# Kernel optimization log

Measured on AMD Instinct MI355X. Metric: run time of the kernel, lower is better.

The kernel has to match this reference:

```python
import jax, jax.numpy as jnp
import numpy as np

D_MODEL = 512  # scale uses sqrt(d_model), faithful to source (not sqrt(d_k))


def setup_inputs() -> dict:
    key = jax.random.key(0)
    ks = jax.random.split(key, 9)
    S, H, DK, DV = 4096, 8, 128, 64
    w = lambda k, shape: jax.random.normal(k, shape, jnp.float32) * 0.02
    return {
        "x": jax.random.normal(ks[0], (S, D_MODEL), jnp.float32),
        "Wq": w(ks[1], (H, D_MODEL, DK)), "bq": w(ks[2], (H, DK)),
        "Wk": w(ks[3], (H, D_MODEL, DK)), "bk": w(ks[4], (H, DK)),
        "Wv": w(ks[5], (H, D_MODEL, DV)), "bv": w(ks[6], (H, DV)),
        "Wo": w(ks[7], (H * DV, D_MODEL)), "bo": w(ks[8], (D_MODEL,)),
    }


def reference(x, Wq, bq, Wk, bk, Wv, bv, Wo, bo):
    # Per-head Q/K/V projections, batched over heads: [H, S, dk/dv]
    q = jnp.einsum('sd,hdk->hsk', x, Wq) + bq[:, None, :]
    k = jnp.einsum('sd,hdk->hsk', x, Wk) + bk[:, None, :]
    v = jnp.einsum('sd,hdv->hsv', x, Wv) + bv[:, None, :]
    # scaled dot-product; source divides by sqrt(d_model), mask branch is a no-op
    scores = jnp.einsum('hsk,htk->hst', q, k) / jnp.sqrt(jnp.float32(D_MODEL))
    probs = jax.nn.softmax(scores, axis=-1)  # softmax(dim=1) on 2D == last axis
    heads = jnp.einsum('hst,htv->hsv', probs, v)          # [H, S, DV]
    concat = jnp.transpose(heads, (1, 0, 2)).reshape(x.shape[0], -1)  # [S, H*DV]
    return concat @ Wo + bo
```

## Files before the change

kernel.cpp:

```cpp
#include <hip/hip_runtime.h>
#include <hip/hip_bf16.h>
#include <math.h>

typedef __bf16 bf16_t;
typedef __bf16 bf16x4 __attribute__((ext_vector_type(4)));
typedef __bf16 bf16x8 __attribute__((ext_vector_type(8)));
typedef float  f32x4  __attribute__((ext_vector_type(4)));

#define LOG2E   1.4426950408889634f
#define QSCALE  0.04419417382415922f
#define QS_TOT  (QSCALE * LOG2E)

static __device__ __forceinline__ f32x4 mfma16(bf16x8 a, bf16x8 b, f32x4 c) {
    return __builtin_amdgcn_mfma_f32_16x16x32_bf16(a, b, c, 0, 0, 0);
}

static __device__ __forceinline__ void gload16(void* lds, const void* g) {
    __builtin_amdgcn_global_load_lds(
        (const __attribute__((address_space(1))) unsigned int*)g,
        (__attribute__((address_space(3))) unsigned int*)lds, 16, 0, 0);
}

__global__ void k_stage_all(const float* __restrict__ x,
                            const float* __restrict__ Wq, const float* __restrict__ Wk,
                            const float* __restrict__ Wv, const float* __restrict__ Wo,
                            const float* __restrict__ bq, const float* __restrict__ bk,
                            const float* __restrict__ bv,
                            bf16_t* __restrict__ xb, bf16_t* __restrict__ Wcat,
                            bf16_t* __restrict__ Wot, float* __restrict__ bcat) {
    __shared__ float tl[64][65];
    int b = blockIdx.x;
    if (b < 2048) {
        int i = (b * 256 + (int)threadIdx.x) * 4;
        f32x4 v = *(const f32x4*)(x + i);
        bf16x4 o;
        o[0] = (bf16_t)v[0]; o[1] = (bf16_t)v[1]; o[2] = (bf16_t)v[2]; o[3] = (bf16_t)v[3];
        *(bf16x4*)(xb + i) = o;
        return;
    }
    if (b < 2432) {
        int bb = b - 2048;
        int p = bb >> 7, bid = bb & 127;
        int h = bid >> 4, rem = bid & 15, dt = rem >> 1, ct = rem & 1;
        if (p == 2 && ct) return;
        int cols = (p == 2) ? 64 : 128;
        const float* src = (p == 0 ? Wq : (p == 1 ? Wk : Wv)) + h * 512 * cols;
        int d0 = dt * 64, c0 = ct * 64;
        int cin = threadIdx.x & 63, rb = threadIdx.x >> 6;
        #pragma unroll
        for (int j = 0; j < 16; j++) {
            int dl = rb * 16 + j;
            tl[dl][cin] = src[(d0 + dl) * cols + c0 + cin];
        }
        __syncthreads();
        float sc = (p == 0) ? QS_TOT : 1.0f;
        int nl = threadIdx.x >> 2, dch = (threadIdx.x & 3) * 16;
        int n = h * 320 + p * 128 + c0 + nl;
        bf16_t* dst = Wcat + n * 512 + d0 + dch;
        #pragma unroll
        for (int e = 0; e < 16; e += 4) {
            bf16x4 o;
            #pragma unroll
            for (int q = 0; q < 4; q++) o[q] = (bf16_t)(tl[dch + e + q][nl] * sc);
            *(bf16x4*)(dst + e) = o;
        }
        return;
    }
    if (b < 2496) {
        int bb = b - 2432;
        int r0 = (bb >> 3) * 64, c0 = (bb & 7) * 64;
        int cin = threadIdx.x & 63, rb = threadIdx.x >> 6;
        #pragma unroll
        for (int j = 0; j < 16; j++) {
            int rl = rb * 16 + j;
            tl[rl][cin] = Wo[(r0 + rl) * 512 + c0 + cin];
        }
        __syncthreads();
        int nl = threadIdx.x >> 2, dch = (threadIdx.x & 3) * 16;
        bf16_t* dst = Wot + (c0 + nl) * 512 + r0 + dch;
        #pragma unroll
        for (int e = 0; e < 16; e += 4) {
            bf16x4 o;
            #pragma unroll
            for (int q = 0; q < 4; q++) o[q] = (bf16_t)tl[dch + e + q][nl];
            *(bf16x4*)(dst + e) = o;
        }
        return;
    }
    {
        int n = (b - 2496) * 256 + (int)threadIdx.x;
        if (n >= 2560) return;
        int h = n / 320, r = n % 320;
        float v;
        if (r < 128)      v = bq[h * 128 + r] * QS_TOT;
        else if (r < 256) v = bk[h * 128 + r - 128];
        else              v = bv[h * 64 + r - 256];
        bcat[n] = v;
    }
}

static __device__ __forceinline__ void stage_tile(bf16_t* lds, const bf16_t* src_base,
                                                  int row0, int kk, int wv, int lane) {
    #pragma unroll
    for (int j = 0; j < 2; ++j) {
        int row = j * 64 + wv * 16 + (lane >> 2);
        int slot = lane & 3;
        const bf16_t* src = src_base + (size_t)(row0 + row) * 512 + kk
                          + ((slot ^ ((row >> 1) & 3)) << 3);
        gload16(lds + (j * 64 + wv * 16) * 32, src);
    }
}

__global__ __launch_bounds__(256) void k_gemm_qkv(
        const bf16_t* __restrict__ xb, const bf16_t* __restrict__ Wcat,
        const float* __restrict__ bcat,
        bf16_t* __restrict__ Qb, bf16_t* __restrict__ Kb, bf16_t* __restrict__ Vt) {
    __shared__ __align__(16) bf16_t a_lds[2][128 * 32];
    __shared__ __align__(16) bf16_t b_lds[2][128 * 32];

    int lane = threadIdx.x & 63, wv = threadIdx.x >> 6;
    int qi = lane & 15, g = lane >> 4;
    int m0 = blockIdx.x * 128;
    int n0 = blockIdx.y * 128;

    f32x4 acc[4][4];
    #pragma unroll
    for (int ar = 0; ar < 4; ar++)
        #pragma unroll
        for (int br = 0; br < 4; br++) acc[ar][br] = (f32x4){0.f,0.f,0.f,0.f};

    int arow0 = (wv >> 1) * 64;
    int brow0 = (wv & 1) * 64;

    stage_tile(&a_lds[0][0], xb,   m0, 0, wv, lane);
    stage_tile(&b_lds[0][0], Wcat, n0, 0, wv, lane);

    for (int t = 0; t < 16; ++t) {
        __syncthreads();
        int cur = t & 1;
        if (t + 1 < 16) {
            stage_tile(&a_lds[cur ^ 1][0], xb,   m0, (t + 1) * 32, wv, lane);
            stage_tile(&b_lds[cur ^ 1][0], Wcat, n0, (t + 1) * 32, wv, lane);
        }
        const char* abase = (const char*)&a_lds[cur][0];
        const char* bbase = (const char*)&b_lds[cur][0];
        bf16x8 af[4], bf[4];
        #pragma unroll
        for (int ar = 0; ar < 4; ar++) {
            int row = arow0 + ar * 16 + qi;
            af[ar] = *(const bf16x8*)(abase + row * 64 + (((g ^ (row >> 1)) & 3) << 4));
        }
        #pragma unroll
        for (int br = 0; br < 4; br++) {
            int row = brow0 + br * 16 + qi;
            bf[br] = *(const bf16x8*)(bbase + row * 64 + (((g ^ (row >> 1)) & 3) << 4));
        }
        __builtin_amdgcn_s_setprio(1);
        #pragma unroll
        for (int ar = 0; ar < 4; ar++)
            #pragma unroll
            for (int br = 0; br < 4; br++)
                acc[ar][br] = mfma16(af[ar], bf[br], acc[ar][br]);
        __builtin_amdgcn_s_setprio(0);
    }

    int mrow = m0 + arow0;
    int ncol = n0 + brow0;
    #pragma unroll
    for (int br = 0; br < 4; br++) {
        int n = ncol + br * 16 + qi;
        float bias = bcat[n];
        int h = n / 320, r = n % 320;
        #pragma unroll
        for (int ar = 0; ar < 4; ar++)
            #pragma unroll
            for (int i = 0; i < 4; i++) {
                int rr = mrow + ar * 16 + g * 4 + i;
                float val = acc[ar][br][i] + bias;
                if (r < 128)      Qb[(h * 4096 + rr) * 128 + r]         = (bf16_t)val;
                else if (r < 256) Kb[(h * 4096 + rr) * 128 + (r - 128)] = (bf16_t)val;
                else {
                    int cp = (rr & ~31) | (((rr >> 2) & 3) << 3) | (((rr >> 4) & 1) << 2) | (rr & 3);
                    Vt[(h * 64 + (r - 256)) * 4096 + cp] = (bf16_t)val;
                }
            }
    }
}

static __device__ __forceinline__ void stage_k(bf16_t* kbuf, const bf16_t* Kh,
                                               int kt, int wv, int lane) {
    #pragma unroll
    for (int j = 0; j < 4; ++j) {
        int local = wv * 16 + j * 4 + (lane >> 4);
        int physcol = (lane & 15) << 4;
        const char* src = (const char*)(Kh + (size_t)(kt + local) * 128)
                        + (physcol ^ ((local & 7) << 4));
        gload16(kbuf + (wv * 16 + j * 4) * 128, src);
    }
}

static __device__ __forceinline__ void stage_v(bf16_t* vbuf, const bf16_t* Vh,
                                               int kt, int wv, int lane) {
    #pragma unroll
    for (int jj = 0; jj < 2; ++jj) {
        int j = wv * 2 + jj;
        int dv = j * 8 + (lane >> 3);
        int slot = lane & 7;
        const bf16_t* src = Vh + (size_t)dv * 4096 + kt + ((slot ^ (dv & 7)) << 3);
        gload16(vbuf + j * 512, src);
    }
}

__global__ __launch_bounds__(256, 3) void k_attn(
        const bf16_t* __restrict__ Qb, const bf16_t* __restrict__ Kb,
        const bf16_t* __restrict__ Vt, bf16_t* __restrict__ Cb,
        float* __restrict__ Opart, float* __restrict__ Lpart) {
    __shared__ __align__(16) bf16_t k_lds[2][64 * 128];
    __shared__ __align__(16) bf16_t v_lds[2][64 * 64];

    const int lane = threadIdx.x & 63, wv = threadIdx.x >> 6;
    const int qi = lane & 15, g = lane >> 4;

    int nwg = 32 * 8 * gridDim.z, cpx = nwg >> 3;
    int wgid = blockIdx.x + 32 * (blockIdx.y + 8 * blockIdx.z);
    int wk = (wgid & 7) * cpx + (wgid >> 3);
    const int qb = wk & 31, h = (wk >> 5) & 7, split = wk >> 8;

    const int nsplits = gridDim.z;
    const int tbase = 64 / nsplits, trem = 64 % nsplits;
    const int tstart = split * tbase + (split < trem ? split : trem);
    const int ntiles = tbase + (split < trem ? 1 : 0);

    const int q0 = qb * 128 + wv * 32;
    int rot = (int)(((unsigned)wgid * 2654435761u) >> 24) % ntiles;

    const bf16_t* Qh = Qb + h * 4096 * 128;
    const bf16_t* Kh = Kb + h * 4096 * 128;
    const bf16_t* Vh = Vt + h * 64 * 4096;

    bf16x8 qf[2][4];
    #pragma unroll
    for (int qt = 0; qt < 2; qt++)
        #pragma unroll
        for (int c = 0; c < 4; c++)
            qf[qt][c] = *(const bf16x8*)(Qh + (q0 + qt * 16 + qi) * 128 + c * 32 + g * 8);

    float l[2] = {0.f, 0.f};
    f32x4 oacc[2][4];
    #pragma unroll
    for (int qt = 0; qt < 2; qt++)
        #pragma unroll
        for (int c = 0; c < 4; c++) oacc[qt][c] = (f32x4){0.f,0.f,0.f,0.f};

    {
        int kt0 = (tstart + rot) * 64;
        stage_k(&k_lds[0][0], Kh, kt0, wv, lane);
        stage_v(&v_lds[0][0], Vh, kt0, wv, lane);
    }
    __syncthreads();

    for (int ii = 0; ii < ntiles; ++ii) {
        const int cur = ii & 1;
        if (ii + 1 < ntiles) {
            int idn = ii + 1 + rot; if (idn >= ntiles) idn -= ntiles;
            int ktn = (tstart + idn) * 64;
            stage_k(&k_lds[cur ^ 1][0], Kh, ktn, wv, lane);
            stage_v(&v_lds[cur ^ 1][0], Vh, ktn, wv, lane);
        }

        f32x4 s[2][4];
        #pragma unroll
        for (int qt = 0; qt < 2; qt++)
            #pragma unroll
            for (int t = 0; t < 4; t++) s[qt][t] = (f32x4){0.f,0.f,0.f,0.f};
        __builtin_amdgcn_s_setprio(1);
        #pragma unroll
        for (int t = 0; t < 4; t++) {
            const bf16_t* kr = &k_lds[cur][(t * 16 + qi) * 128];
            #pragma unroll
            for (int c = 0; c < 4; c++) {
                int offb = (c * 64 + g * 16) ^ ((qi & 7) << 4);
                bf16x8 kf = *(const bf16x8*)(kr + (offb >> 1));
                s[0][t] = mfma16(kf, qf[0][c], s[0][t]);
                s[1][t] = mfma16(kf, qf[1][c], s[1][t]);
            }
        }
        __builtin_amdgcn_s_setprio(0);

        float p[2][4][4];
        #pragma unroll
        for (int qt = 0; qt < 2; qt++) {
            float ks = 0.f;
            #pragma unroll
            for (int t = 0; t < 4; t++)
                #pragma unroll
                for (int i = 0; i < 4; i++) {
                    float e = __builtin_amdgcn_exp2f(s[qt][t][i]);
                    p[qt][t][i] = e;
                    ks += e;
                }
            l[qt] += ks;
        }

        bf16x8 pb[2][2];
        #pragma unroll
        for (int qt = 0; qt < 2; qt++)
            #pragma unroll
            for (int u = 0; u < 2; u++) {
                bf16x8 t8;
                #pragma unroll
                for (int e = 0; e < 4; e++) {
                    t8[e]     = (bf16_t)p[qt][2 * u][e];
                    t8[4 + e] = (bf16_t)p[qt][2 * u + 1][e];
                }
                pb[qt][u] = t8;
            }

        __builtin_amdgcn_s_setprio(1);
        #pragma unroll
        for (int c = 0; c < 4; c++) {
            const char* vrow = (const char*)&v_lds[cur][0] + (c * 16 + qi) * 128;
            #pragma unroll
            for (int u = 0; u < 2; u++) {
                int offb = (g * 16 + u * 64) ^ ((qi & 7) << 4);
                bf16x8 vf = *(const bf16x8*)(vrow + offb);
                oacc[0][c] = mfma16(vf, pb[0][u], oacc[0][c]);
                oacc[1][c] = mfma16(vf, pb[1][u], oacc[1][c]);
            }
        }
        __builtin_amdgcn_s_setprio(0);

        __syncthreads();
    }

    #pragma unroll
    for (int qt = 0; qt < 2; qt++) {
        l[qt] += __shfl_xor(l[qt], 16);
        l[qt] += __shfl_xor(l[qt], 32);
    }

    if (gridDim.z == 1) {
        #pragma unroll
        for (int qt = 0; qt < 2; qt++) {
            float inv = 1.0f / l[qt];
            int q = q0 + qt * 16 + qi;
            #pragma unroll
            for (int c = 0; c < 4; c++) {
                bf16x4 o4;
                #pragma unroll
                for (int i = 0; i < 4; i++) o4[i] = (bf16_t)(oacc[qt][c][i] * inv);
                *(bf16x4*)(Cb + q * 512 + h * 64 + c * 16 + g * 4) = o4;
            }
        }
    } else {
        #pragma unroll
        for (int qt = 0; qt < 2; qt++) {
            int q = q0 + qt * 16 + qi;
            float* Op = Opart + ((size_t)(split * 8 + h) * 4096 + q) * 64;
            #pragma unroll
            for (int c = 0; c < 4; c++)
                *(f32x4*)(Op + c * 16 + g * 4) = oacc[qt][c];
            if (g == 0)
                Lpart[(size_t)(split * 8 + h) * 4096 + q] = l[qt];
        }
    }
}

__global__ void k_merge(const float* __restrict__ Opart, const float* __restrict__ Lpart,
                        bf16_t* __restrict__ Cb, int splits) {
    int idx = blockIdx.x * 256 + threadIdx.x;
    int q = idx >> 7, rem = idx & 127;
    int hv4 = rem * 4;
    int h = hv4 >> 6, dv = hv4 & 63;

    f32x4 acc = {0.f, 0.f, 0.f, 0.f};
    float L = 0.f;
    for (int s = 0; s < splits; s++) {
        L += Lpart[(size_t)(s * 8 + h) * 4096 + q];
        f32x4 ov = *(const f32x4*)(Opart + ((size_t)(s * 8 + h) * 4096 + q) * 64 + dv);
        #pragma unroll
        for (int e = 0; e < 4; e++) acc[e] += ov[e];
    }
    float inv = 1.0f / L;
    bf16x4 o4;
    #pragma unroll
    for (int e = 0; e < 4; e++) o4[e] = (bf16_t)(acc[e] * inv);
    *(bf16x4*)(Cb + (size_t)q * 512 + hv4) = o4;
}

__global__ __launch_bounds__(256) void k_gemm_out(
        const bf16_t* __restrict__ Cb, const bf16_t* __restrict__ Wot,
        const float* __restrict__ bo, float* __restrict__ out) {
    __shared__ __align__(16) bf16_t a_lds[2][128 * 32];
    __shared__ __align__(16) bf16_t b_lds[2][128 * 32];

    int lane = threadIdx.x & 63, wv = threadIdx.x >> 6;
    int qi = lane & 15, g = lane >> 4;
    int m0 = blockIdx.x * 128;
    int n0 = blockIdx.y * 128;

    f32x4 acc[4][4];
    #pragma unroll
    for (int ar = 0; ar < 4; ar++)
        #pragma unroll
        for (int br = 0; br < 4; br++) acc[ar][br] = (f32x4){0.f,0.f,0.f,0.f};

    int arow0 = (wv >> 1) * 64;
    int brow0 = (wv & 1) * 64;

    stage_tile(&a_lds[0][0], Cb,  m0, 0, wv, lane);
    stage_tile(&b_lds[0][0], Wot, n0, 0, wv, lane);

    for (int t = 0; t < 16; ++t) {
        __syncthreads();
        int cur = t & 1;
        if (t + 1 < 16) {
            stage_tile(&a_lds[cur ^ 1][0], Cb,  m0, (t + 1) * 32, wv, lane);
            stage_tile(&b_lds[cur ^ 1][0], Wot, n0, (t + 1) * 32, wv, lane);
        }
        const char* abase = (const char*)&a_lds[cur][0];
        const char* bbase = (const char*)&b_lds[cur][0];
        bf16x8 af[4], bf[4];
        #pragma unroll
        for (int ar = 0; ar < 4; ar++) {
            int row = arow0 + ar * 16 + qi;
            af[ar] = *(const bf16x8*)(abase + row * 64 + (((g ^ (row >> 1)) & 3) << 4));
        }
        #pragma unroll
        for (int br = 0; br < 4; br++) {
            int row = brow0 + br * 16 + qi;
            bf[br] = *(const bf16x8*)(bbase + row * 64 + (((g ^ (row >> 1)) & 3) << 4));
        }
        __builtin_amdgcn_s_setprio(1);
        #pragma unroll
        for (int ar = 0; ar < 4; ar++)
            #pragma unroll
            for (int br = 0; br < 4; br++)
                acc[ar][br] = mfma16(af[ar], bf[br], acc[ar][br]);
        __builtin_amdgcn_s_setprio(0);
    }

    int mrow = m0 + arow0;
    int ncol = n0 + brow0;
    #pragma unroll
    for (int br = 0; br < 4; br++) {
        int n = ncol + br * 16 + qi;
        float bias = bo[n];
        #pragma unroll
        for (int ar = 0; ar < 4; ar++)
            #pragma unroll
            for (int i = 0; i < 4; i++)
                out[(mrow + ar * 16 + g * 4 + i) * 512 + n] = acc[ar][br][i] + bias;
    }
}

extern "C" void kernel_launch(void* const* d_in, const int* in_sizes, int n_in,
                              void* d_out, int out_size, void* d_ws, size_t ws_size,
                              hipStream_t stream) {
    const float* x  = (const float*)d_in[0];
    const float* Wq = (const float*)d_in[1];
    const float* bq = (const float*)d_in[2];
    const float* Wk = (const float*)d_in[3];
    const float* bk = (const float*)d_in[4];
    const float* Wv = (const float*)d_in[5];
    const float* bv = (const float*)d_in[6];
    const float* Wo = (const float*)d_in[7];
    const float* bo = (const float*)d_in[8];
    float* out = (float*)d_out;

    char* ws = (char*)d_ws;
    bf16_t* xb    = (bf16_t*)(ws + 0);
    bf16_t* Wcat  = (bf16_t*)(ws + 4194304);
    bf16_t* Qb    = (bf16_t*)(ws + 6815744);
    bf16_t* Kb    = (bf16_t*)(ws + 15204352);
    bf16_t* Vt    = (bf16_t*)(ws + 23592960);
    bf16_t* Cb    = (bf16_t*)(ws + 27787264);
    bf16_t* Wot   = (bf16_t*)(ws + 31981568);
    float*  bcat  = (float*)(ws + 32505856);
    float*  Opart = (float*)(ws + 32516096);
    float*  Lprt  = (float*)(ws + 57681920);
    const size_t NEED3 = 58075136;
    int splits = (ws_size >= NEED3) ? 3 : 1;

    hipLaunchKernelGGL(k_stage_all,  dim3(2506),   dim3(256), 0, stream,
                       x, Wq, Wk, Wv, Wo, bq, bk, bv, xb, Wcat, Wot, bcat);
    hipLaunchKernelGGL(k_gemm_qkv,   dim3(32, 20), dim3(256), 0, stream, xb, Wcat, bcat, Qb, Kb, Vt);
    hipLaunchKernelGGL(k_attn,       dim3(32, 8, splits), dim3(256), 0, stream, Qb, Kb, Vt, Cb, Opart, Lprt);
    if (splits > 1)
        hipLaunchKernelGGL(k_merge,  dim3(2048),   dim3(256), 0, stream, Opart, Lprt, Cb, splits);
    hipLaunchKernelGGL(k_gemm_out,   dim3(32, 4),  dim3(256), 0, stream, Cb, Wot, bo, out);
}
```

Measured before the change: 110.9 us.

## Single-buffer V tile to fit four attention blocks per CU, use four KV splits

V staging in the attention kernel goes from double-buffered to single-buffered, which cuts LDS per block. That lets the launch bound rise from 3 to 4 blocks per CU. V fragments are now read into registers before an added barrier, and the next V tile is loaded afterwards, overlapping with the PV MFMAs. The host uses four KV splits when the workspace is large enough and moves the partial-L buffer to make room. The cost is an extra barrier per tile, less prefetch depth for V, and more partial results to merge.

```diff
diff --git a/kernel.cpp b/kernel.cpp
--- a/kernel.cpp
+++ b/kernel.cpp
@@ -211,12 +211,12 @@
     }
 }
 
-__global__ __launch_bounds__(256, 3) void k_attn(
+__global__ __launch_bounds__(256, 4) void k_attn(
         const bf16_t* __restrict__ Qb, const bf16_t* __restrict__ Kb,
         const bf16_t* __restrict__ Vt, bf16_t* __restrict__ Cb,
         float* __restrict__ Opart, float* __restrict__ Lpart) {
     __shared__ __align__(16) bf16_t k_lds[2][64 * 128];
-    __shared__ __align__(16) bf16_t v_lds[2][64 * 64];
+    __shared__ __align__(16) bf16_t v_lds[64 * 64];
 
     const int lane = threadIdx.x & 63, wv = threadIdx.x >> 6;
     const int qi = lane & 15, g = lane >> 4;
@@ -255,17 +255,18 @@
     {
         int kt0 = (tstart + rot) * 64;
         stage_k(&k_lds[0][0], Kh, kt0, wv, lane);
-        stage_v(&v_lds[0][0], Vh, kt0, wv, lane);
+        stage_v(&v_lds[0], Vh, kt0, wv, lane);
     }
     __syncthreads();
 
     for (int ii = 0; ii < ntiles; ++ii) {
         const int cur = ii & 1;
-        if (ii + 1 < ntiles) {
+        int ktn = 0;
+        const bool more = (ii + 1 < ntiles);
+        if (more) {
             int idn = ii + 1 + rot; if (idn >= ntiles) idn -= ntiles;
-            int ktn = (tstart + idn) * 64;
+            ktn = (tstart + idn) * 64;
             stage_k(&k_lds[cur ^ 1][0], Kh, ktn, wv, lane);
-            stage_v(&v_lds[cur ^ 1][0], Vh, ktn, wv, lane);
         }
 
         f32x4 s[2][4];
@@ -316,18 +317,28 @@
                 pb[qt][u] = t8;
             }
 
-        __builtin_amdgcn_s_setprio(1);
+        bf16x8 vf[4][2];
         #pragma unroll
         for (int c = 0; c < 4; c++) {
-            const char* vrow = (const char*)&v_lds[cur][0] + (c * 16 + qi) * 128;
+            const char* vrow = (const char*)&v_lds[0] + (c * 16 + qi) * 128;
             #pragma unroll
             for (int u = 0; u < 2; u++) {
                 int offb = (g * 16 + u * 64) ^ ((qi & 7) << 4);
-                bf16x8 vf = *(const bf16x8*)(vrow + offb);
-                oacc[0][c] = mfma16(vf, pb[0][u], oacc[0][c]);
-                oacc[1][c] = mfma16(vf, pb[1][u], oacc[1][c]);
+                vf[c][u] = *(const bf16x8*)(vrow + offb);
             }
         }
+        __syncthreads();
+
+        if (more) stage_v(&v_lds[0], Vh, ktn, wv, lane);
+
+        __builtin_amdgcn_s_setprio(1);
+        #pragma unroll
+        for (int c = 0; c < 4; c++)
+            #pragma unroll
+            for (int u = 0; u < 2; u++) {
+                oacc[0][c] = mfma16(vf[c][u], pb[0][u], oacc[0][c]);
+                oacc[1][c] = mfma16(vf[c][u], pb[1][u], oacc[1][c]);
+            }
         __builtin_amdgcn_s_setprio(0);
 
         __syncthreads();
@@ -478,9 +489,10 @@
     bf16_t* Wot   = (bf16_t*)(ws + 31981568);
     float*  bcat  = (float*)(ws + 32505856);
     float*  Opart = (float*)(ws + 32516096);
-    float*  Lprt  = (float*)(ws + 57681920);
+    float*  Lprt  = (float*)(ws + 66070528);
+    const size_t NEED4 = 67119104;
     const size_t NEED3 = 58075136;
-    int splits = (ws_size >= NEED3) ? 3 : 1;
+    int splits = (ws_size >= NEED4) ? 4 : ((ws_size >= NEED3) ? 3 : 1);
 
     hipLaunchKernelGGL(k_stage_all,  dim3(2506),   dim3(256), 0, stream,
                        x, Wq, Wk, Wv, Wo, bq, bk, bv, xb, Wcat, Wot, bcat);
```

Result: slower. 263.7 us (+137.8%).

## Software-pipeline PV matmul one tile behind QK with triple-buffered V

Applied to the files above, without the earlier changes.

Restructures the attention loop so the P·V MFMAs for the previous tile are issued right after the current tile's QK^T MFMAs, overlapping the exp/softmax work with matrix work. V staging moves to a three-slot LDS ring so the lagged tile stays resident, and a final epilogue drains the last P·V. It also drops the occupancy hint of three blocks per SM and reduces KV splits from 3 to 2. This adds LDS and register pressure, which may lower occupancy.

```diff
diff --git a/kernel.cpp b/kernel.cpp
--- a/kernel.cpp
+++ b/kernel.cpp
@@ -211,12 +211,12 @@
     }
 }
 
-__global__ __launch_bounds__(256, 3) void k_attn(
+__global__ __launch_bounds__(256) void k_attn(
         const bf16_t* __restrict__ Qb, const bf16_t* __restrict__ Kb,
         const bf16_t* __restrict__ Vt, bf16_t* __restrict__ Cb,
         float* __restrict__ Opart, float* __restrict__ Lpart) {
     __shared__ __align__(16) bf16_t k_lds[2][64 * 128];
-    __shared__ __align__(16) bf16_t v_lds[2][64 * 64];
+    __shared__ __align__(16) bf16_t v_lds[3][64 * 64];
 
     const int lane = threadIdx.x & 63, wv = threadIdx.x >> 6;
     const int qi = lane & 15, g = lane >> 4;
@@ -252,6 +252,8 @@
         #pragma unroll
         for (int c = 0; c < 4; c++) oacc[qt][c] = (f32x4){0.f,0.f,0.f,0.f};
 
+    bf16x8 pbp[2][2];
+
     {
         int kt0 = (tstart + rot) * 64;
         stage_k(&k_lds[0][0], Kh, kt0, wv, lane);
@@ -259,13 +261,17 @@
     }
     __syncthreads();
 
+    int bc = 0;
     for (int ii = 0; ii < ntiles; ++ii) {
-        const int cur = ii & 1;
+        const int kcur = ii & 1;
+        int bn = bc + 1; if (bn == 3) bn = 0;
+        int bp = bn + 1; if (bp == 3) bp = 0;
+
         if (ii + 1 < ntiles) {
             int idn = ii + 1 + rot; if (idn >= ntiles) idn -= ntiles;
             int ktn = (tstart + idn) * 64;
-            stage_k(&k_lds[cur ^ 1][0], Kh, ktn, wv, lane);
-            stage_v(&v_lds[cur ^ 1][0], Vh, ktn, wv, lane);
+            stage_k(&k_lds[kcur ^ 1][0], Kh, ktn, wv, lane);
+            stage_v(&v_lds[bn][0], Vh, ktn, wv, lane);
         }
 
         f32x4 s[2][4];
@@ -276,13 +282,27 @@
         __builtin_amdgcn_s_setprio(1);
         #pragma unroll
         for (int t = 0; t < 4; t++) {
-            const bf16_t* kr = &k_lds[cur][(t * 16 + qi) * 128];
+            const bf16_t* kr = &k_lds[kcur][(t * 16 + qi) * 128];
             #pragma unroll
             for (int c = 0; c < 4; c++) {
                 int offb = (c * 64 + g * 16) ^ ((qi & 7) << 4);
                 bf16x8 kf = *(const bf16x8*)(kr + (offb >> 1));
                 s[0][t] = mfma16(kf, qf[0][c], s[0][t]);
                 s[1][t] = mfma16(kf, qf[1][c], s[1][t]);
+            }
+        }
+
+        if (ii > 0) {
+            #pragma unroll
+            for (int c = 0; c < 4; c++) {
+                const char* vrow = (const char*)&v_lds[bp][0] + (c * 16 + qi) * 128;
+                #pragma unroll
+                for (int u = 0; u < 2; u++) {
+                    int offb = (g * 16 + u * 64) ^ ((qi & 7) << 4);
+                    bf16x8 vf = *(const bf16x8*)(vrow + offb);
+                    oacc[0][c] = mfma16(vf, pbp[0][u], oacc[0][c]);
+                    oacc[1][c] = mfma16(vf, pbp[1][u], oacc[1][c]);
+                }
             }
         }
         __builtin_amdgcn_s_setprio(0);
@@ -302,7 +322,6 @@
             l[qt] += ks;
         }
 
-        bf16x8 pb[2][2];
         #pragma unroll
         for (int qt = 0; qt < 2; qt++)
             #pragma unroll
@@ -313,24 +332,28 @@
                     t8[e]     = (bf16_t)p[qt][2 * u][e];
                     t8[4 + e] = (bf16_t)p[qt][2 * u + 1][e];
                 }
-                pb[qt][u] = t8;
+                pbp[qt][u] = t8;
             }
 
+        bc = bn;
+        __syncthreads();
+    }
+
+    {
+        int bl = bc + 2; if (bl >= 3) bl -= 3;
         __builtin_amdgcn_s_setprio(1);
         #pragma unroll
         for (int c = 0; c < 4; c++) {
-            const char* vrow = (const char*)&v_lds[cur][0] + (c * 16 + qi) * 128;
+            const char* vrow = (const char*)&v_lds[bl][0] + (c * 16 + qi) * 128;
             #pragma unroll
             for (int u = 0; u < 2; u++) {
                 int offb = (g * 16 + u * 64) ^ ((qi & 7) << 4);
                 bf16x8 vf = *(const bf16x8*)(vrow + offb);
-                oacc[0][c] = mfma16(vf, pb[0][u], oacc[0][c]);
-                oacc[1][c] = mfma16(vf, pb[1][u], oacc[1][c]);
+                oacc[0][c] = mfma16(vf, pbp[0][u], oacc[0][c]);
+                oacc[1][c] = mfma16(vf, pbp[1][u], oacc[1][c]);
             }
         }
         __builtin_amdgcn_s_setprio(0);
-
-        __syncthreads();
     }
 
     #pragma unroll
@@ -478,9 +501,9 @@
     bf16_t* Wot   = (bf16_t*)(ws + 31981568);
     float*  bcat  = (float*)(ws + 32505856);
     float*  Opart = (float*)(ws + 32516096);
-    float*  Lprt  = (float*)(ws + 57681920);
-    const size_t NEED3 = 58075136;
-    int splits = (ws_size >= NEED3) ? 3 : 1;
+    float*  Lprt  = (float*)(ws + 49293312);
+    const size_t NEED2 = 49555456;
+    int splits = (ws_size >= NEED2) ? 2 : 1;
 
     hipLaunchKernelGGL(k_stage_all,  dim3(2506),   dim3(256), 0, stream,
                        x, Wq, Wk, Wv, Wo, bq, bk, bv, xb, Wcat, Wot, bcat);
```

New measurement: 108.3 us. -2.3%, faster.
